# Kernel tuning notes

Measured on AMD Instinct MI355X. Metric: run time of the kernel, lower is better.

Reference implementation:

```python
import jax, jax.numpy as jnp
import numpy as np

HIDDEN = 2048
NUM_HEAD = 32
GROUP = 8
HEAD_DIM = HIDDEN // NUM_HEAD  # 64
REP = NUM_HEAD // GROUP        # 4


def setup_inputs() -> dict:
    key = jax.random.key(0)
    ks = jax.random.split(key, 9)
    s = 0.02
    kv_dim = GROUP * HEAD_DIM
    return {
        "hidden_states": jax.random.normal(ks[0], (2, 2048, HIDDEN), dtype=jnp.float32),
        "Wq": jax.random.normal(ks[1], (HIDDEN, HIDDEN), dtype=jnp.float32) * s,
        "bq": jnp.zeros((HIDDEN,), dtype=jnp.float32),
        "Wk": jax.random.normal(ks[2], (HIDDEN, kv_dim), dtype=jnp.float32) * s,
        "bk": jnp.zeros((kv_dim,), dtype=jnp.float32),
        "Wv": jax.random.normal(ks[3], (HIDDEN, kv_dim), dtype=jnp.float32) * s,
        "bv": jnp.zeros((kv_dim,), dtype=jnp.float32),
        "Wo": jax.random.normal(ks[4], (HIDDEN, HIDDEN), dtype=jnp.float32) * s,
        "bo": jnp.zeros((HIDDEN,), dtype=jnp.float32),
    }


def reference(hidden_states, Wq, bq, Wk, bk, Wv, bv, Wo, bo):
    B, S, H = hidden_states.shape
    q = hidden_states @ Wq + bq                      # [B,S,H]
    k = hidden_states @ Wk + bk                      # [B,S,G*hd]
    v = hidden_states @ Wv + bv
    q = q.reshape(B, S, NUM_HEAD, HEAD_DIM).transpose(0, 2, 1, 3)   # [B,nh,S,hd]
    k = k.reshape(B, S, GROUP, HEAD_DIM).transpose(0, 2, 1, 3)      # [B,G,S,hd]
    v = v.reshape(B, S, GROUP, HEAD_DIM).transpose(0, 2, 1, 3)
    # expand KV heads: each group head repeated REP times contiguously
    k = jnp.repeat(k, REP, axis=1)                   # [B,nh,S,hd]
    v = jnp.repeat(v, REP, axis=1)
    scale = 1.0 / jnp.sqrt(jnp.float32(HEAD_DIM))
    scores = jnp.einsum("bhqd,bhkd->bhqk", q, k) * scale  # [B,nh,S,S]
    attn = jax.nn.softmax(scores, axis=-1)
    out = jnp.einsum("bhqk,bhkd->bhqd", attn, v)     # [B,nh,S,hd]
    out = out.transpose(0, 2, 1, 3).reshape(B, S, NUM_HEAD * HEAD_DIM)
    return out @ Wo + bo
```

## Files before the change

kernel.cpp:

```cpp
#include <hip/hip_runtime.h>
#include <hip/hip_bf16.h>

typedef __attribute__((ext_vector_type(8))) short bf16x8;
typedef __attribute__((ext_vector_type(4))) short bf16x4;
typedef __attribute__((ext_vector_type(4))) float f32x4;

__device__ __forceinline__ unsigned short f2bf(float f) {
  union { float f; unsigned int u; } v; v.f = f;
  unsigned int r = (v.u + 0x7fffu + ((v.u >> 16) & 1u)) >> 16;
  return (unsigned short)r;
}

__device__ __forceinline__ unsigned int pk2bf(float a, float b) {
  float2 t; t.x = a; t.y = b;
  __hip_bfloat162 h = __float22bfloat162_rn(t);
  union { __hip_bfloat162 h; unsigned int u; } cv; cv.h = h;
  return cv.u;
}

__device__ __forceinline__ void g2l16(unsigned short* lds, const unsigned short* g) {
  __builtin_amdgcn_global_load_lds(
      (const __attribute__((address_space(1))) unsigned int*)g,
      (__attribute__((address_space(3))) unsigned int*)lds, 16, 0, 0);
}


__global__ __launch_bounds__(256) void cast_hs_kernel(const float* __restrict__ in,
                                                      unsigned short* __restrict__ out) {
  size_t i = (size_t)blockIdx.x * 256 + threadIdx.x;
  float4 v = ((const float4*)in)[i];
  ushort4 o;
  o.x = f2bf(v.x); o.y = f2bf(v.y); o.z = f2bf(v.z); o.w = f2bf(v.w);
  ((ushort4*)out)[i] = o;
}

__global__ __launch_bounds__(256) void transpose_all_kernel(
    const float* __restrict__ Wq, const float* __restrict__ Wk,
    const float* __restrict__ Wv, const float* __restrict__ Wo,
    unsigned short* __restrict__ Wqkv, unsigned short* __restrict__ WoT) {
  __shared__ float tile[32][33];
  int z = blockIdx.z;
  const float* src; unsigned short* dst; int N;
  if (z == 0)      { src = Wq; dst = Wqkv;                          N = 2048; }
  else if (z == 1) { src = Wk; dst = Wqkv + (size_t)2048 * 2048;    N = 512; }
  else if (z == 2) { src = Wv; dst = Wqkv + (size_t)2560 * 2048;    N = 512; }
  else             { src = Wo; dst = WoT;                           N = 2048; }
  if (blockIdx.x * 32 >= N) return;
  int n0 = blockIdx.x * 32, k0 = blockIdx.y * 32;
  int t = threadIdx.x;
  for (int i = 0; i < 4; ++i) {
    int linear = i * 256 + t;
    int kr = linear >> 5, nc = linear & 31;
    tile[kr][nc] = src[(size_t)(k0 + kr) * N + (n0 + nc)];
  }
  __syncthreads();
  for (int i = 0; i < 4; ++i) {
    int linear = i * 256 + t;
    int nr = linear >> 5, kc = linear & 31;
    dst[(size_t)(n0 + nr) * 2048 + (k0 + kc)] = f2bf(tile[kc][nr]);
  }
}


#define QSCALE 0.18033688011112042f

__global__ __launch_bounds__(256) void gemm_qkv_kernel(
    const unsigned short* __restrict__ A, const unsigned short* __restrict__ Bt,
    const float* __restrict__ bq, const float* __restrict__ bk, const float* __restrict__ bv,
    unsigned short* __restrict__ Qb, unsigned short* __restrict__ Kb,
    unsigned short* __restrict__ Vtb) {
  __shared__ __align__(16) unsigned short smem[128 * 136];
  unsigned short* sA = smem;
  unsigned short* sB = smem + 4096;
  const int K = 2048;
  int bm0 = blockIdx.y * 128, bn0 = blockIdx.x * 128;
  int t = threadIdx.x;
  int w = t >> 6, lane = t & 63, l16 = lane & 15, quad = lane >> 4;
  int wm = (w & 1) * 64, wn = (w >> 1) * 64;
  f32x4 zero = {0.f, 0.f, 0.f, 0.f};
  f32x4 acc[4][4];
  for (int mt = 0; mt < 4; ++mt)
    for (int nt = 0; nt < 4; ++nt) acc[mt][nt] = zero;

  for (int k0 = 0; k0 < K; k0 += 32) {
    for (int i = 0; i < 2; ++i) {
      int linear = i * 256 + t;
      int row = linear >> 2, kofs = (linear & 3) * 8;
      g2l16(sA + linear * 8, A + (size_t)(bm0 + row) * K + k0 + kofs);
      g2l16(sB + linear * 8, Bt + (size_t)(bn0 + row) * K + k0 + kofs);
    }
    __syncthreads();
    bf16x8 af[4], bfr[4];
    for (int mt = 0; mt < 4; ++mt)
      af[mt] = *(const bf16x8*)(sA + (wm + mt * 16 + l16) * 32 + quad * 8);
    for (int nt = 0; nt < 4; ++nt)
      bfr[nt] = *(const bf16x8*)(sB + (wn + nt * 16 + l16) * 32 + quad * 8);
    for (int mt = 0; mt < 4; ++mt)
      for (int nt = 0; nt < 4; ++nt)
        acc[mt][nt] = __builtin_amdgcn_mfma_f32_16x16x32_bf16(af[mt], bfr[nt], acc[mt][nt], 0, 0, 0);
    __syncthreads();
  }

  const int SP = 136;
  bool isV = (bn0 >= 2560);
  bool isQ = (bn0 < 2048);
  const float* bias = isQ ? bq : (bn0 < 2560 ? bk : bv);
  int nbase = isQ ? 0 : (bn0 < 2560 ? 2048 : 2560);

  for (int nt = 0; nt < 4; ++nt) {
    int nl = wn + nt * 16 + l16;
    float bb = bias[bn0 + nl - nbase];
    for (int mt = 0; mt < 4; ++mt)
      for (int r = 0; r < 4; ++r) {
        int ml = wm + mt * 16 + quad * 4 + r;
        float fv = acc[mt][nt][r] + bb;
        if (isQ) fv *= QSCALE;
        unsigned short val = f2bf(fv);
        if (isV) smem[nl * SP + ml] = val;
        else     smem[ml * SP + nl] = val;
      }
  }
  __syncthreads();

  int b = bm0 >> 11, s0 = bm0 & 2047;
  if (bn0 < 2048) {
    for (int i = 0; i < 8; ++i) {
      int idx = i * 256 + t;
      int sub = idx >> 10, s_l = (idx >> 3) & 127, dch = (idx & 7) * 8;
      bf16x8 v = *(const bf16x8*)(smem + s_l * SP + sub * 64 + dch);
      int n = bn0 + sub * 64 + dch;
      int h = n >> 6, d = n & 63;
      *(bf16x8*)(Qb + (((size_t)b * 32 + h) * 2048 + s0 + s_l) * 64 + d) = v;
    }
  } else if (bn0 < 2560) {
    for (int i = 0; i < 8; ++i) {
      int idx = i * 256 + t;
      int sub = idx >> 10, s_l = (idx >> 3) & 127, dch = (idx & 7) * 8;
      bf16x8 v = *(const bf16x8*)(smem + s_l * SP + sub * 64 + dch);
      int nn = bn0 + sub * 64 + dch - 2048;
      int g = nn >> 6, d = nn & 63;
      *(bf16x8*)(Kb + (((size_t)b * 8 + g) * 2048 + s0 + s_l) * 64 + d) = v;
    }
  } else {
    for (int i = 0; i < 8; ++i) {
      int idx = i * 256 + t;
      int nl = idx >> 4, sj = (idx & 15) * 8;
      bf16x8 v = *(const bf16x8*)(smem + nl * SP + sj);
      int nn = bn0 + nl - 2560;
      int g = nn >> 6, d = nn & 63;
      *(bf16x8*)(Vtb + (((size_t)b * 8 + g) * 64 + d) * 2048 + s0 + sj) = v;
    }
  }
}


__global__ __launch_bounds__(256) void attn_kernel(
    const unsigned short* __restrict__ Qb, const unsigned short* __restrict__ Kb,
    const unsigned short* __restrict__ Vtb, unsigned short* __restrict__ AttnB) {
  __shared__ __align__(16) unsigned short Kt[64 * 64];
  __shared__ __align__(16) unsigned short Vt[64 * 64];
  int qt = blockIdx.x, h = blockIdx.y, b = blockIdx.z;
  int g = h >> 2;
  int t = threadIdx.x, w = t >> 6, lane = t & 63, l16 = lane & 15, quad = lane >> 4;

  const unsigned short* qb0 =
      Qb + (((size_t)b * 32 + h) * 2048 + qt * 128 + w * 16 + l16) * 64 + quad * 8;
  const unsigned short* qb1 = qb0 + (size_t)64 * 64;
  bf16x8 aQ0a = *(const bf16x8*)(qb0);
  bf16x8 aQ1a = *(const bf16x8*)(qb0 + 32);
  bf16x8 aQ0b = *(const bf16x8*)(qb1);
  bf16x8 aQ1b = *(const bf16x8*)(qb1 + 32);

  const unsigned short* kbase = Kb + ((size_t)b * 8 + g) * (2048 * 64);
  const unsigned short* vbase = Vtb + ((size_t)b * 8 + g) * (64 * 2048);

  f32x4 zero = {0.f, 0.f, 0.f, 0.f};
  f32x4 m10 = {-10.f, -10.f, -10.f, -10.f};
  union { unsigned short s[4]; bf16x4 v; } ones;
  ones.s[0] = 0x3F80; ones.s[1] = 0x3F80; ones.s[2] = 0x3F80; ones.s[3] = 0x3F80;

  f32x4 oA[4], oB[4], olA, olB;
  for (int dt = 0; dt < 4; ++dt) { oA[dt] = zero; oB[dt] = zero; }
  olA = zero; olB = zero;

  for (int kb = 0; kb < 32; ++kb) {
    for (int i = 0; i < 2; ++i) {
      int linear = i * 256 + t;
      int row = linear & 63, c = linear >> 6;
      g2l16(Kt + linear * 8, kbase + (size_t)(kb * 64 + row) * 64 + c * 8);
      g2l16(Vt + linear * 8, vbase + (size_t)row * 2048 + kb * 64 + c * 8);
    }
    __syncthreads();

    for (int nt = 0; nt < 4; ++nt) {
      bf16x8 bk0 = *(const bf16x8*)(Kt + (quad * 64 + nt * 16 + l16) * 8);
      bf16x8 bk1 = *(const bf16x8*)(Kt + ((quad + 4) * 64 + nt * 16 + l16) * 8);
      f32x4 stA = __builtin_amdgcn_mfma_f32_16x16x32_bf16(bk0, aQ0a, m10, 0, 0, 0);
      stA = __builtin_amdgcn_mfma_f32_16x16x32_bf16(bk1, aQ1a, stA, 0, 0, 0);
      f32x4 stB = __builtin_amdgcn_mfma_f32_16x16x32_bf16(bk0, aQ0b, m10, 0, 0, 0);
      stB = __builtin_amdgcn_mfma_f32_16x16x32_bf16(bk1, aQ1b, stB, 0, 0, 0);

      union { unsigned int u[2]; bf16x4 v; } paA, paB;
      paA.u[0] = pk2bf(__builtin_amdgcn_exp2f(stA[0]), __builtin_amdgcn_exp2f(stA[1]));
      paA.u[1] = pk2bf(__builtin_amdgcn_exp2f(stA[2]), __builtin_amdgcn_exp2f(stA[3]));
      paB.u[0] = pk2bf(__builtin_amdgcn_exp2f(stB[0]), __builtin_amdgcn_exp2f(stB[1]));
      paB.u[1] = pk2bf(__builtin_amdgcn_exp2f(stB[2]), __builtin_amdgcn_exp2f(stB[3]));

      olA = __builtin_amdgcn_mfma_f32_16x16x16bf16_1k(paA.v, ones.v, olA, 0, 0, 0);
      olB = __builtin_amdgcn_mfma_f32_16x16x16bf16_1k(paB.v, ones.v, olB, 0, 0, 0);

      int c = nt * 2 + (quad >> 1);
      int ho = (quad & 1) * 4;
      for (int dt = 0; dt < 4; ++dt) {
        bf16x4 bv = *(const bf16x4*)(Vt + (c * 64 + dt * 16 + l16) * 8 + ho);
        oA[dt] = __builtin_amdgcn_mfma_f32_16x16x16bf16_1k(paA.v, bv, oA[dt], 0, 0, 0);
        oB[dt] = __builtin_amdgcn_mfma_f32_16x16x16bf16_1k(paB.v, bv, oB[dt], 0, 0, 0);
      }
    }
    __syncthreads();
  }

  for (int r = 0; r < 4; ++r) {
    float invA = 1.f / olA[r];
    float invB = 1.f / olB[r];
    int srow0 = qt * 128 + w * 16 + quad * 4 + r;
    size_t base0 = ((size_t)b * 2048 + srow0) * 2048 + h * 64;
    size_t base1 = base0 + (size_t)64 * 2048;
    for (int dt = 0; dt < 4; ++dt) {
      AttnB[base0 + dt * 16 + l16] = f2bf(oA[dt][r] * invA);
      AttnB[base1 + dt * 16 + l16] = f2bf(oB[dt][r] * invB);
    }
  }
}


__global__ __launch_bounds__(256) void gemm_out_kernel(
    const unsigned short* __restrict__ A, const unsigned short* __restrict__ Bt,
    const float* __restrict__ bo, float* __restrict__ out) {
  __shared__ __align__(16) unsigned short sA[128 * 32];
  __shared__ __align__(16) unsigned short sB[128 * 32];
  const int K = 2048;
  int bm0 = blockIdx.y * 128, bn0 = blockIdx.x * 128;
  int t = threadIdx.x;
  int w = t >> 6, lane = t & 63, l16 = lane & 15, quad = lane >> 4;
  int wm = (w & 1) * 64, wn = (w >> 1) * 64;
  f32x4 zero = {0.f, 0.f, 0.f, 0.f};
  f32x4 acc[4][4];
  for (int mt = 0; mt < 4; ++mt)
    for (int nt = 0; nt < 4; ++nt) acc[mt][nt] = zero;

  for (int k0 = 0; k0 < K; k0 += 32) {
    for (int i = 0; i < 2; ++i) {
      int linear = i * 256 + t;
      int row = linear >> 2, kofs = (linear & 3) * 8;
      g2l16(sA + linear * 8, A + (size_t)(bm0 + row) * K + k0 + kofs);
      g2l16(sB + linear * 8, Bt + (size_t)(bn0 + row) * K + k0 + kofs);
    }
    __syncthreads();
    bf16x8 af[4], bfr[4];
    for (int mt = 0; mt < 4; ++mt)
      af[mt] = *(const bf16x8*)(sA + (wm + mt * 16 + l16) * 32 + quad * 8);
    for (int nt = 0; nt < 4; ++nt)
      bfr[nt] = *(const bf16x8*)(sB + (wn + nt * 16 + l16) * 32 + quad * 8);
    for (int mt = 0; mt < 4; ++mt)
      for (int nt = 0; nt < 4; ++nt)
        acc[mt][nt] = __builtin_amdgcn_mfma_f32_16x16x32_bf16(af[mt], bfr[nt], acc[mt][nt], 0, 0, 0);
    __syncthreads();
  }

  for (int nt = 0; nt < 4; ++nt) {
    int n = bn0 + wn + nt * 16 + l16;
    float bias = bo[n];
    for (int mt = 0; mt < 4; ++mt)
      for (int r = 0; r < 4; ++r) {
        int m = bm0 + wm + mt * 16 + quad * 4 + r;
        out[(size_t)m * 2048 + n] = acc[mt][nt][r] + bias;
      }
  }
}


extern "C" void kernel_launch(void* const* d_in, const int* in_sizes, int n_in,
                              void* d_out, int out_size, void* d_ws, size_t ws_size,
                              hipStream_t stream) {
  const float* hs = (const float*)d_in[0];
  const float* Wq = (const float*)d_in[1];
  const float* bq = (const float*)d_in[2];
  const float* Wk = (const float*)d_in[3];
  const float* bk = (const float*)d_in[4];
  const float* Wv = (const float*)d_in[5];
  const float* bv = (const float*)d_in[6];
  const float* Wo = (const float*)d_in[7];
  const float* bo = (const float*)d_in[8];
  float* out = (float*)d_out;

  char* ws = (char*)d_ws;
  unsigned short* hsb   = (unsigned short*)(ws);
  unsigned short* Wqkv  = (unsigned short*)(ws + 16777216);
  unsigned short* WoT   = (unsigned short*)(ws + 29360128);
  unsigned short* Qb    = (unsigned short*)(ws + 37748736);
  unsigned short* Kb    = (unsigned short*)(ws + 54525952);
  unsigned short* Vtb   = (unsigned short*)(ws + 58720256);
  unsigned short* AttnB = (unsigned short*)(ws + 62914560);

  hipLaunchKernelGGL(cast_hs_kernel, dim3(8192), dim3(256), 0, stream, hs, hsb);
  hipLaunchKernelGGL(transpose_all_kernel, dim3(64, 64, 4), dim3(256), 0, stream,
                     Wq, Wk, Wv, Wo, Wqkv, WoT);
  hipLaunchKernelGGL(gemm_qkv_kernel, dim3(24, 32), dim3(256), 0, stream,
                     hsb, Wqkv, bq, bk, bv, Qb, Kb, Vtb);
  hipLaunchKernelGGL(attn_kernel, dim3(16, 32, 2), dim3(256), 0, stream, Qb, Kb, Vtb, AttnB);
  hipLaunchKernelGGL(gemm_out_kernel, dim3(16, 32), dim3(256), 0, stream, AttnB, WoT, bo, out);
}
```

Measured before the change: 343.0 us.

## Double-buffer attention K/V tiles and widen GEMM K-step to 64

```diff
diff --git a/kernel.cpp b/kernel.cpp
--- a/kernel.cpp
+++ b/kernel.cpp
@@ -71,7 +71,7 @@
     unsigned short* __restrict__ Vtb) {
   __shared__ __align__(16) unsigned short smem[128 * 136];
   unsigned short* sA = smem;
-  unsigned short* sB = smem + 4096;
+  unsigned short* sB = smem + 8192;
   const int K = 2048;
   int bm0 = blockIdx.y * 128, bn0 = blockIdx.x * 128;
   int t = threadIdx.x;
@@ -82,22 +82,24 @@
   for (int mt = 0; mt < 4; ++mt)
     for (int nt = 0; nt < 4; ++nt) acc[mt][nt] = zero;
 
-  for (int k0 = 0; k0 < K; k0 += 32) {
-    for (int i = 0; i < 2; ++i) {
+  for (int k0 = 0; k0 < K; k0 += 64) {
+    for (int i = 0; i < 4; ++i) {
       int linear = i * 256 + t;
-      int row = linear >> 2, kofs = (linear & 3) * 8;
+      int row = linear >> 3, kofs = (linear & 7) * 8;
       g2l16(sA + linear * 8, A + (size_t)(bm0 + row) * K + k0 + kofs);
       g2l16(sB + linear * 8, Bt + (size_t)(bn0 + row) * K + k0 + kofs);
     }
     __syncthreads();
-    bf16x8 af[4], bfr[4];
-    for (int mt = 0; mt < 4; ++mt)
-      af[mt] = *(const bf16x8*)(sA + (wm + mt * 16 + l16) * 32 + quad * 8);
-    for (int nt = 0; nt < 4; ++nt)
-      bfr[nt] = *(const bf16x8*)(sB + (wn + nt * 16 + l16) * 32 + quad * 8);
-    for (int mt = 0; mt < 4; ++mt)
+    for (int kk = 0; kk < 2; ++kk) {
+      bf16x8 af[4], bfr[4];
+      for (int mt = 0; mt < 4; ++mt)
+        af[mt] = *(const bf16x8*)(sA + (wm + mt * 16 + l16) * 64 + kk * 32 + quad * 8);
       for (int nt = 0; nt < 4; ++nt)
-        acc[mt][nt] = __builtin_amdgcn_mfma_f32_16x16x32_bf16(af[mt], bfr[nt], acc[mt][nt], 0, 0, 0);
+        bfr[nt] = *(const bf16x8*)(sB + (wn + nt * 16 + l16) * 64 + kk * 32 + quad * 8);
+      for (int mt = 0; mt < 4; ++mt)
+        for (int nt = 0; nt < 4; ++nt)
+          acc[mt][nt] = __builtin_amdgcn_mfma_f32_16x16x32_bf16(af[mt], bfr[nt], acc[mt][nt], 0, 0, 0);
+    }
     __syncthreads();
   }
 
@@ -157,8 +159,8 @@
 __global__ __launch_bounds__(256) void attn_kernel(
     const unsigned short* __restrict__ Qb, const unsigned short* __restrict__ Kb,
     const unsigned short* __restrict__ Vtb, unsigned short* __restrict__ AttnB) {
-  __shared__ __align__(16) unsigned short Kt[64 * 64];
-  __shared__ __align__(16) unsigned short Vt[64 * 64];
+  __shared__ __align__(16) unsigned short Kt[2][64 * 64];
+  __shared__ __align__(16) unsigned short Vt[2][64 * 64];
   int qt = blockIdx.x, h = blockIdx.y, b = blockIdx.z;
   int g = h >> 2;
   int t = threadIdx.x, w = t >> 6, lane = t & 63, l16 = lane & 15, quad = lane >> 4;
@@ -174,6 +176,15 @@
   const unsigned short* kbase = Kb + ((size_t)b * 8 + g) * (2048 * 64);
   const unsigned short* vbase = Vtb + ((size_t)b * 8 + g) * (64 * 2048);
 
+  auto stage = [&](int buf, int kb) {
+    for (int i = 0; i < 2; ++i) {
+      int linear = i * 256 + t;
+      int row = linear & 63, c = linear >> 6;
+      g2l16(&Kt[buf][linear * 8], kbase + (size_t)(kb * 64 + row) * 64 + c * 8);
+      g2l16(&Vt[buf][linear * 8], vbase + (size_t)row * 2048 + kb * 64 + c * 8);
+    }
+  };
+
   f32x4 zero = {0.f, 0.f, 0.f, 0.f};
   f32x4 m10 = {-10.f, -10.f, -10.f, -10.f};
   union { unsigned short s[4]; bf16x4 v; } ones;
@@ -183,22 +194,24 @@
   for (int dt = 0; dt < 4; ++dt) { oA[dt] = zero; oB[dt] = zero; }
   olA = zero; olB = zero;
 
+  stage(0, 0);
+  __syncthreads();
+
+  int cur = 0;
   for (int kb = 0; kb < 32; ++kb) {
-    for (int i = 0; i < 2; ++i) {
-      int linear = i * 256 + t;
-      int row = linear & 63, c = linear >> 6;
-      g2l16(Kt + linear * 8, kbase + (size_t)(kb * 64 + row) * 64 + c * 8);
-      g2l16(Vt + linear * 8, vbase + (size_t)row * 2048 + kb * 64 + c * 8);
-    }
-    __syncthreads();
+    if (kb < 31) stage(cur ^ 1, kb + 1);
+    const unsigned short* Kc = &Kt[cur][0];
+    const unsigned short* Vc = &Vt[cur][0];
 
     for (int nt = 0; nt < 4; ++nt) {
-      bf16x8 bk0 = *(const bf16x8*)(Kt + (quad * 64 + nt * 16 + l16) * 8);
-      bf16x8 bk1 = *(const bf16x8*)(Kt + ((quad + 4) * 64 + nt * 16 + l16) * 8);
+      bf16x8 bk0 = *(const bf16x8*)(Kc + (quad * 64 + nt * 16 + l16) * 8);
+      bf16x8 bk1 = *(const bf16x8*)(Kc + ((quad + 4) * 64 + nt * 16 + l16) * 8);
+      __builtin_amdgcn_s_setprio(1);
       f32x4 stA = __builtin_amdgcn_mfma_f32_16x16x32_bf16(bk0, aQ0a, m10, 0, 0, 0);
       stA = __builtin_amdgcn_mfma_f32_16x16x32_bf16(bk1, aQ1a, stA, 0, 0, 0);
       f32x4 stB = __builtin_amdgcn_mfma_f32_16x16x32_bf16(bk0, aQ0b, m10, 0, 0, 0);
       stB = __builtin_amdgcn_mfma_f32_16x16x32_bf16(bk1, aQ1b, stB, 0, 0, 0);
+      __builtin_amdgcn_s_setprio(0);
 
       union { unsigned int u[2]; bf16x4 v; } paA, paB;
       paA.u[0] = pk2bf(__builtin_amdgcn_exp2f(stA[0]), __builtin_amdgcn_exp2f(stA[1]));
@@ -206,18 +219,21 @@
       paB.u[0] = pk2bf(__builtin_amdgcn_exp2f(stB[0]), __builtin_amdgcn_exp2f(stB[1]));
       paB.u[1] = pk2bf(__builtin_amdgcn_exp2f(stB[2]), __builtin_amdgcn_exp2f(stB[3]));
 
+      __builtin_amdgcn_s_setprio(1);
       olA = __builtin_amdgcn_mfma_f32_16x16x16bf16_1k(paA.v, ones.v, olA, 0, 0, 0);
       olB = __builtin_amdgcn_mfma_f32_16x16x16bf16_1k(paB.v, ones.v, olB, 0, 0, 0);
 
       int c = nt * 2 + (quad >> 1);
       int ho = (quad & 1) * 4;
       for (int dt = 0; dt < 4; ++dt) {
-        bf16x4 bv = *(const bf16x4*)(Vt + (c * 64 + dt * 16 + l16) * 8 + ho);
+        bf16x4 bv = *(const bf16x4*)(Vc + (c * 64 + dt * 16 + l16) * 8 + ho);
         oA[dt] = __builtin_amdgcn_mfma_f32_16x16x16bf16_1k(paA.v, bv, oA[dt], 0, 0, 0);
         oB[dt] = __builtin_amdgcn_mfma_f32_16x16x16bf16_1k(paB.v, bv, oB[dt], 0, 0, 0);
       }
-    }
-    __syncthreads();
+      __builtin_amdgcn_s_setprio(0);
+    }
+    __syncthreads();
+    cur ^= 1;
   }
 
   for (int r = 0; r < 4; ++r) {
@@ -237,8 +253,8 @@
 __global__ __launch_bounds__(256) void gemm_out_kernel(
     const unsigned short* __restrict__ A, const unsigned short* __restrict__ Bt,
     const float* __restrict__ bo, float* __restrict__ out) {
-  __shared__ __align__(16) unsigned short sA[128 * 32];
-  __shared__ __align__(16) unsigned short sB[128 * 32];
+  __shared__ __align__(16) unsigned short sA[128 * 64];
+  __shared__ __align__(16) unsigned short sB[128 * 64];
   const int K = 2048;
   int bm0 = blockIdx.y * 128, bn0 = blockIdx.x * 128;
   int t = threadIdx.x;
@@ -249,22 +265,24 @@
   for (int mt = 0; mt < 4; ++mt)
     for (int nt = 0; nt < 4; ++nt) acc[mt][nt] = zero;
 
-  for (int k0 = 0; k0 < K; k0 += 32) {
-    for (int i = 0; i < 2; ++i) {
+  for (int k0 = 0; k0 < K; k0 += 64) {
+    for (int i = 0; i < 4; ++i) {
       int linear = i * 256 + t;
-      int row = linear >> 2, kofs = (linear & 3) * 8;
+      int row = linear >> 3, kofs = (linear & 7) * 8;
       g2l16(sA + linear * 8, A + (size_t)(bm0 + row) * K + k0 + kofs);
       g2l16(sB + linear * 8, Bt + (size_t)(bn0 + row) * K + k0 + kofs);
     }
     __syncthreads();
-    bf16x8 af[4], bfr[4];
-    for (int mt = 0; mt < 4; ++mt)
-      af[mt] = *(const bf16x8*)(sA + (wm + mt * 16 + l16) * 32 + quad * 8);
-    for (int nt = 0; nt < 4; ++nt)
-      bfr[nt] = *(const bf16x8*)(sB + (wn + nt * 16 + l16) * 32 + quad * 8);
-    for (int mt = 0; mt < 4; ++mt)
+    for (int kk = 0; kk < 2; ++kk) {
+      bf16x8 af[4], bfr[4];
+      for (int mt = 0; mt < 4; ++mt)
+        af[mt] = *(const bf16x8*)(sA + (wm + mt * 16 + l16) * 64 + kk * 32 + quad * 8);
       for (int nt = 0; nt < 4; ++nt)
-        acc[mt][nt] = __builtin_amdgcn_mfma_f32_16x16x32_bf16(af[mt], bfr[nt], acc[mt][nt], 0, 0, 0);
+        bfr[nt] = *(const bf16x8*)(sB + (wn + nt * 16 + l16) * 64 + kk * 32 + quad * 8);
+      for (int mt = 0; mt < 4; ++mt)
+        for (int nt = 0; nt < 4; ++nt)
+          acc[mt][nt] = __builtin_amdgcn_mfma_f32_16x16x32_bf16(af[mt], bfr[nt], acc[mt][nt], 0, 0, 0);
+    }
     __syncthreads();
   }
 
```

Result: slower. 398.8 us (+16.3%).

## Widen GEMM K-tile to 64 with XOR-swizzled LDS and register-prefetch attention K/V

Applied to the files above, without the earlier changes.

```diff
diff --git a/kernel.cpp b/kernel.cpp
--- a/kernel.cpp
+++ b/kernel.cpp
@@ -71,7 +71,7 @@
     unsigned short* __restrict__ Vtb) {
   __shared__ __align__(16) unsigned short smem[128 * 136];
   unsigned short* sA = smem;
-  unsigned short* sB = smem + 4096;
+  unsigned short* sB = smem + 8192;
   const int K = 2048;
   int bm0 = blockIdx.y * 128, bn0 = blockIdx.x * 128;
   int t = threadIdx.x;
@@ -82,22 +82,29 @@
   for (int mt = 0; mt < 4; ++mt)
     for (int nt = 0; nt < 4; ++nt) acc[mt][nt] = zero;
 
-  for (int k0 = 0; k0 < K; k0 += 32) {
-    for (int i = 0; i < 2; ++i) {
+  for (int k0 = 0; k0 < K; k0 += 64) {
+    for (int i = 0; i < 4; ++i) {
       int linear = i * 256 + t;
-      int row = linear >> 2, kofs = (linear & 3) * 8;
+      int row = linear >> 3, ch = linear & 7;
+      int kofs = (ch ^ (row & 7)) * 8;
       g2l16(sA + linear * 8, A + (size_t)(bm0 + row) * K + k0 + kofs);
       g2l16(sB + linear * 8, Bt + (size_t)(bn0 + row) * K + k0 + kofs);
     }
     __syncthreads();
-    bf16x8 af[4], bfr[4];
-    for (int mt = 0; mt < 4; ++mt)
-      af[mt] = *(const bf16x8*)(sA + (wm + mt * 16 + l16) * 32 + quad * 8);
-    for (int nt = 0; nt < 4; ++nt)
-      bfr[nt] = *(const bf16x8*)(sB + (wn + nt * 16 + l16) * 32 + quad * 8);
-    for (int mt = 0; mt < 4; ++mt)
-      for (int nt = 0; nt < 4; ++nt)
-        acc[mt][nt] = __builtin_amdgcn_mfma_f32_16x16x32_bf16(af[mt], bfr[nt], acc[mt][nt], 0, 0, 0);
+    for (int kk = 0; kk < 2; ++kk) {
+      bf16x8 af[4], bfr[4];
+      for (int mt = 0; mt < 4; ++mt) {
+        int r = wm + mt * 16 + l16;
+        af[mt] = *(const bf16x8*)(sA + r * 64 + ((kk * 4 + quad) ^ (r & 7)) * 8);
+      }
+      for (int nt = 0; nt < 4; ++nt) {
+        int r = wn + nt * 16 + l16;
+        bfr[nt] = *(const bf16x8*)(sB + r * 64 + ((kk * 4 + quad) ^ (r & 7)) * 8);
+      }
+      for (int mt = 0; mt < 4; ++mt)
+        for (int nt = 0; nt < 4; ++nt)
+          acc[mt][nt] = __builtin_amdgcn_mfma_f32_16x16x32_bf16(af[mt], bfr[nt], acc[mt][nt], 0, 0, 0);
+    }
     __syncthreads();
   }
 
@@ -174,6 +181,21 @@
   const unsigned short* kbase = Kb + ((size_t)b * 8 + g) * (2048 * 64);
   const unsigned short* vbase = Vtb + ((size_t)b * 8 + g) * (64 * 2048);
 
+  int lin0 = t, lin1 = 256 + t;
+  int r0 = lin0 & 63, c0 = lin0 >> 6;
+  int r1 = lin1 & 63, c1 = lin1 >> 6;
+  const unsigned short* gK0 = kbase + (size_t)r0 * 64 + c0 * 8;
+  const unsigned short* gK1 = kbase + (size_t)r1 * 64 + c1 * 8;
+  const unsigned short* gV0 = vbase + (size_t)r0 * 2048 + c0 * 8;
+  const unsigned short* gV1 = vbase + (size_t)r1 * 2048 + c1 * 8;
+  unsigned short* wK0 = Kt + lin0 * 8;
+  unsigned short* wK1 = Kt + lin1 * 8;
+  unsigned short* wV0 = Vt + lin0 * 8;
+  unsigned short* wV1 = Vt + lin1 * 8;
+  int sw0 = (c0 & 1) * 4, sw1 = (c1 & 1) * 4;
+
+  union u8 { bf16x8 v; bf16x4 h[2]; };
+
   f32x4 zero = {0.f, 0.f, 0.f, 0.f};
   f32x4 m10 = {-10.f, -10.f, -10.f, -10.f};
   union { unsigned short s[4]; bf16x4 v; } ones;
@@ -183,14 +205,29 @@
   for (int dt = 0; dt < 4; ++dt) { oA[dt] = zero; oB[dt] = zero; }
   olA = zero; olB = zero;
 
+  int pho = ((quad ^ (quad >> 1)) & 1) * 4;
+
+  {
+    bf16x8 rk0 = *(const bf16x8*)(gK0);
+    bf16x8 rk1 = *(const bf16x8*)(gK1);
+    union u8 rv0, rv1; rv0.v = *(const bf16x8*)(gV0); rv1.v = *(const bf16x8*)(gV1);
+    *(bf16x8*)wK0 = rk0;
+    *(bf16x8*)wK1 = rk1;
+    *(bf16x4*)(wV0 + sw0) = rv0.h[0];
+    *(bf16x4*)(wV0 + (sw0 ^ 4)) = rv0.h[1];
+    *(bf16x4*)(wV1 + sw1) = rv1.h[0];
+    *(bf16x4*)(wV1 + (sw1 ^ 4)) = rv1.h[1];
+  }
+  __syncthreads();
+
   for (int kb = 0; kb < 32; ++kb) {
-    for (int i = 0; i < 2; ++i) {
-      int linear = i * 256 + t;
-      int row = linear & 63, c = linear >> 6;
-      g2l16(Kt + linear * 8, kbase + (size_t)(kb * 64 + row) * 64 + c * 8);
-      g2l16(Vt + linear * 8, vbase + (size_t)row * 2048 + kb * 64 + c * 8);
-    }
-    __syncthreads();
+    bf16x8 rk0, rk1; union u8 rv0, rv1;
+    if (kb < 31) {
+      rk0 = *(const bf16x8*)(gK0 + (size_t)(kb + 1) * 4096);
+      rk1 = *(const bf16x8*)(gK1 + (size_t)(kb + 1) * 4096);
+      rv0.v = *(const bf16x8*)(gV0 + (size_t)(kb + 1) * 64);
+      rv1.v = *(const bf16x8*)(gV1 + (size_t)(kb + 1) * 64);
+    }
 
     for (int nt = 0; nt < 4; ++nt) {
       bf16x8 bk0 = *(const bf16x8*)(Kt + (quad * 64 + nt * 16 + l16) * 8);
@@ -210,12 +247,20 @@
       olB = __builtin_amdgcn_mfma_f32_16x16x16bf16_1k(paB.v, ones.v, olB, 0, 0, 0);
 
       int c = nt * 2 + (quad >> 1);
-      int ho = (quad & 1) * 4;
       for (int dt = 0; dt < 4; ++dt) {
-        bf16x4 bv = *(const bf16x4*)(Vt + (c * 64 + dt * 16 + l16) * 8 + ho);
+        bf16x4 bv = *(const bf16x4*)(Vt + (c * 64 + dt * 16 + l16) * 8 + pho);
         oA[dt] = __builtin_amdgcn_mfma_f32_16x16x16bf16_1k(paA.v, bv, oA[dt], 0, 0, 0);
         oB[dt] = __builtin_amdgcn_mfma_f32_16x16x16bf16_1k(paB.v, bv, oB[dt], 0, 0, 0);
       }
+    }
+    __syncthreads();
+    if (kb < 31) {
+      *(bf16x8*)wK0 = rk0;
+      *(bf16x8*)wK1 = rk1;
+      *(bf16x4*)(wV0 + sw0) = rv0.h[0];
+      *(bf16x4*)(wV0 + (sw0 ^ 4)) = rv0.h[1];
+      *(bf16x4*)(wV1 + sw1) = rv1.h[0];
+      *(bf16x4*)(wV1 + (sw1 ^ 4)) = rv1.h[1];
     }
     __syncthreads();
   }
@@ -237,8 +282,8 @@
 __global__ __launch_bounds__(256) void gemm_out_kernel(
     const unsigned short* __restrict__ A, const unsigned short* __restrict__ Bt,
     const float* __restrict__ bo, float* __restrict__ out) {
-  __shared__ __align__(16) unsigned short sA[128 * 32];
-  __shared__ __align__(16) unsigned short sB[128 * 32];
+  __shared__ __align__(16) unsigned short sA[128 * 64];
+  __shared__ __align__(16) unsigned short sB[128 * 64];
   const int K = 2048;
   int bm0 = blockIdx.y * 128, bn0 = blockIdx.x * 128;
   int t = threadIdx.x;
@@ -249,22 +294,29 @@
   for (int mt = 0; mt < 4; ++mt)
     for (int nt = 0; nt < 4; ++nt) acc[mt][nt] = zero;
 
-  for (int k0 = 0; k0 < K; k0 += 32) {
-    for (int i = 0; i < 2; ++i) {
+  for (int k0 = 0; k0 < K; k0 += 64) {
+    for (int i = 0; i < 4; ++i) {
       int linear = i * 256 + t;
-      int row = linear >> 2, kofs = (linear & 3) * 8;
+      int row = linear >> 3, ch = linear & 7;
+      int kofs = (ch ^ (row & 7)) * 8;
       g2l16(sA + linear * 8, A + (size_t)(bm0 + row) * K + k0 + kofs);
       g2l16(sB + linear * 8, Bt + (size_t)(bn0 + row) * K + k0 + kofs);
     }
     __syncthreads();
-    bf16x8 af[4], bfr[4];
-    for (int mt = 0; mt < 4; ++mt)
-      af[mt] = *(const bf16x8*)(sA + (wm + mt * 16 + l16) * 32 + quad * 8);
-    for (int nt = 0; nt < 4; ++nt)
-      bfr[nt] = *(const bf16x8*)(sB + (wn + nt * 16 + l16) * 32 + quad * 8);
-    for (int mt = 0; mt < 4; ++mt)
-      for (int nt = 0; nt < 4; ++nt)
-        acc[mt][nt] = __builtin_amdgcn_mfma_f32_16x16x32_bf16(af[mt], bfr[nt], acc[mt][nt], 0, 0, 0);
+    for (int kk = 0; kk < 2; ++kk) {
+      bf16x8 af[4], bfr[4];
+      for (int mt = 0; mt < 4; ++mt) {
+        int r = wm + mt * 16 + l16;
+        af[mt] = *(const bf16x8*)(sA + r * 64 + ((kk * 4 + quad) ^ (r & 7)) * 8);
+      }
+      for (int nt = 0; nt < 4; ++nt) {
+        int r = wn + nt * 16 + l16;
+        bfr[nt] = *(const bf16x8*)(sB + r * 64 + ((kk * 4 + quad) ^ (r & 7)) * 8);
+      }
+      for (int mt = 0; mt < 4; ++mt)
+        for (int nt = 0; nt < 4; ++nt)
+          acc[mt][nt] = __builtin_amdgcn_mfma_f32_16x16x32_bf16(af[mt], bfr[nt], acc[mt][nt], 0, 0, 0);
+    }
     __syncthreads();
   }
 
```

Result: slower. 352.4 us (+2.8%).

## Split attention work over 8 waves with one query tile per wave

Applied to the files above, without the earlier changes.

```diff
diff --git a/kernel.cpp b/kernel.cpp
--- a/kernel.cpp
+++ b/kernel.cpp
@@ -154,7 +154,7 @@
 }
 
 
-__global__ __launch_bounds__(256) void attn_kernel(
+__global__ __launch_bounds__(512, 8) void attn_kernel(
     const unsigned short* __restrict__ Qb, const unsigned short* __restrict__ Kb,
     const unsigned short* __restrict__ Vtb, unsigned short* __restrict__ AttnB) {
   __shared__ __align__(16) unsigned short Kt[64 * 64];
@@ -163,73 +163,61 @@
   int g = h >> 2;
   int t = threadIdx.x, w = t >> 6, lane = t & 63, l16 = lane & 15, quad = lane >> 4;
 
-  const unsigned short* qb0 =
+  const unsigned short* qb =
       Qb + (((size_t)b * 32 + h) * 2048 + qt * 128 + w * 16 + l16) * 64 + quad * 8;
-  const unsigned short* qb1 = qb0 + (size_t)64 * 64;
-  bf16x8 aQ0a = *(const bf16x8*)(qb0);
-  bf16x8 aQ1a = *(const bf16x8*)(qb0 + 32);
-  bf16x8 aQ0b = *(const bf16x8*)(qb1);
-  bf16x8 aQ1b = *(const bf16x8*)(qb1 + 32);
+  bf16x8 aQ0 = *(const bf16x8*)(qb);
+  bf16x8 aQ1 = *(const bf16x8*)(qb + 32);
 
   const unsigned short* kbase = Kb + ((size_t)b * 8 + g) * (2048 * 64);
   const unsigned short* vbase = Vtb + ((size_t)b * 8 + g) * (64 * 2048);
+  int r_ = t & 63, c_ = t >> 6;
+  const unsigned short* gK = kbase + (size_t)r_ * 64 + c_ * 8;
+  const unsigned short* gV = vbase + (size_t)r_ * 2048 + c_ * 8;
+  unsigned short* wK = Kt + t * 8;
+  unsigned short* wV = Vt + t * 8;
 
   f32x4 zero = {0.f, 0.f, 0.f, 0.f};
   f32x4 m10 = {-10.f, -10.f, -10.f, -10.f};
   union { unsigned short s[4]; bf16x4 v; } ones;
   ones.s[0] = 0x3F80; ones.s[1] = 0x3F80; ones.s[2] = 0x3F80; ones.s[3] = 0x3F80;
 
-  f32x4 oA[4], oB[4], olA, olB;
-  for (int dt = 0; dt < 4; ++dt) { oA[dt] = zero; oB[dt] = zero; }
-  olA = zero; olB = zero;
+  f32x4 oA[4], olA;
+  for (int dt = 0; dt < 4; ++dt) oA[dt] = zero;
+  olA = zero;
 
   for (int kb = 0; kb < 32; ++kb) {
-    for (int i = 0; i < 2; ++i) {
-      int linear = i * 256 + t;
-      int row = linear & 63, c = linear >> 6;
-      g2l16(Kt + linear * 8, kbase + (size_t)(kb * 64 + row) * 64 + c * 8);
-      g2l16(Vt + linear * 8, vbase + (size_t)row * 2048 + kb * 64 + c * 8);
-    }
+    g2l16(wK, gK + (size_t)kb * 4096);
+    g2l16(wV, gV + (size_t)kb * 64);
     __syncthreads();
 
     for (int nt = 0; nt < 4; ++nt) {
       bf16x8 bk0 = *(const bf16x8*)(Kt + (quad * 64 + nt * 16 + l16) * 8);
       bf16x8 bk1 = *(const bf16x8*)(Kt + ((quad + 4) * 64 + nt * 16 + l16) * 8);
-      f32x4 stA = __builtin_amdgcn_mfma_f32_16x16x32_bf16(bk0, aQ0a, m10, 0, 0, 0);
-      stA = __builtin_amdgcn_mfma_f32_16x16x32_bf16(bk1, aQ1a, stA, 0, 0, 0);
-      f32x4 stB = __builtin_amdgcn_mfma_f32_16x16x32_bf16(bk0, aQ0b, m10, 0, 0, 0);
-      stB = __builtin_amdgcn_mfma_f32_16x16x32_bf16(bk1, aQ1b, stB, 0, 0, 0);
-
-      union { unsigned int u[2]; bf16x4 v; } paA, paB;
-      paA.u[0] = pk2bf(__builtin_amdgcn_exp2f(stA[0]), __builtin_amdgcn_exp2f(stA[1]));
-      paA.u[1] = pk2bf(__builtin_amdgcn_exp2f(stA[2]), __builtin_amdgcn_exp2f(stA[3]));
-      paB.u[0] = pk2bf(__builtin_amdgcn_exp2f(stB[0]), __builtin_amdgcn_exp2f(stB[1]));
-      paB.u[1] = pk2bf(__builtin_amdgcn_exp2f(stB[2]), __builtin_amdgcn_exp2f(stB[3]));
-
-      olA = __builtin_amdgcn_mfma_f32_16x16x16bf16_1k(paA.v, ones.v, olA, 0, 0, 0);
-      olB = __builtin_amdgcn_mfma_f32_16x16x16bf16_1k(paB.v, ones.v, olB, 0, 0, 0);
+      f32x4 st = __builtin_amdgcn_mfma_f32_16x16x32_bf16(bk0, aQ0, m10, 0, 0, 0);
+      st = __builtin_amdgcn_mfma_f32_16x16x32_bf16(bk1, aQ1, st, 0, 0, 0);
+
+      union { unsigned int u[2]; bf16x4 v; } pa;
+      pa.u[0] = pk2bf(__builtin_amdgcn_exp2f(st[0]), __builtin_amdgcn_exp2f(st[1]));
+      pa.u[1] = pk2bf(__builtin_amdgcn_exp2f(st[2]), __builtin_amdgcn_exp2f(st[3]));
+
+      olA = __builtin_amdgcn_mfma_f32_16x16x16bf16_1k(pa.v, ones.v, olA, 0, 0, 0);
 
       int c = nt * 2 + (quad >> 1);
       int ho = (quad & 1) * 4;
       for (int dt = 0; dt < 4; ++dt) {
         bf16x4 bv = *(const bf16x4*)(Vt + (c * 64 + dt * 16 + l16) * 8 + ho);
-        oA[dt] = __builtin_amdgcn_mfma_f32_16x16x16bf16_1k(paA.v, bv, oA[dt], 0, 0, 0);
-        oB[dt] = __builtin_amdgcn_mfma_f32_16x16x16bf16_1k(paB.v, bv, oB[dt], 0, 0, 0);
+        oA[dt] = __builtin_amdgcn_mfma_f32_16x16x16bf16_1k(pa.v, bv, oA[dt], 0, 0, 0);
       }
     }
     __syncthreads();
   }
 
   for (int r = 0; r < 4; ++r) {
-    float invA = 1.f / olA[r];
-    float invB = 1.f / olB[r];
-    int srow0 = qt * 128 + w * 16 + quad * 4 + r;
-    size_t base0 = ((size_t)b * 2048 + srow0) * 2048 + h * 64;
-    size_t base1 = base0 + (size_t)64 * 2048;
-    for (int dt = 0; dt < 4; ++dt) {
-      AttnB[base0 + dt * 16 + l16] = f2bf(oA[dt][r] * invA);
-      AttnB[base1 + dt * 16 + l16] = f2bf(oB[dt][r] * invB);
-    }
+    float inv = 1.f / olA[r];
+    int srow = qt * 128 + w * 16 + quad * 4 + r;
+    size_t base = ((size_t)b * 2048 + srow) * 2048 + h * 64;
+    for (int dt = 0; dt < 4; ++dt)
+      AttnB[base + dt * 16 + l16] = f2bf(oA[dt][r] * inv);
   }
 }
 
@@ -308,6 +296,6 @@
                      Wq, Wk, Wv, Wo, Wqkv, WoT);
   hipLaunchKernelGGL(gemm_qkv_kernel, dim3(24, 32), dim3(256), 0, stream,
                      hsb, Wqkv, bq, bk, bv, Qb, Kb, Vtb);
-  hipLaunchKernelGGL(attn_kernel, dim3(16, 32, 2), dim3(256), 0, stream, Qb, Kb, Vtb, AttnB);
+  hipLaunchKernelGGL(attn_kernel, dim3(16, 32, 2), dim3(512), 0, stream, Qb, Kb, Vtb, AttnB);
   hipLaunchKernelGGL(gemm_out_kernel, dim3(16, 32), dim3(256), 0, stream, AttnB, WoT, bo, out);
 }
```

Result: faster. 335.3 us (-2.2%).
